# Performance work log

Measured on AMD Instinct MI355X. Metric: run time of the kernel, lower is better.

The kernel has to match this reference:

```python
import jax, jax.numpy as jnp
import numpy as np

B, S, H, UNITS = 32, 2048, 1024, 1024


def setup_inputs() -> dict:
    key = jax.random.key(0)
    ks = jax.random.split(key, 5)
    scale = 1.0 / np.sqrt(H)
    return {
        "query": jax.random.normal(ks[0], (B, H), dtype=jnp.float32),
        "values": jax.random.normal(ks[1], (B, S, H), dtype=jnp.float32),
        "W1": jax.random.normal(ks[2], (H, UNITS), dtype=jnp.float32) * scale,
        "b1": jnp.zeros((UNITS,), dtype=jnp.float32),
        "W2": jax.random.normal(ks[3], (H, UNITS), dtype=jnp.float32) * scale,
        "b2": jnp.zeros((UNITS,), dtype=jnp.float32),
        "V": jax.random.normal(ks[4], (UNITS, 1), dtype=jnp.float32) * (1.0 / np.sqrt(UNITS)),
        "bV": jnp.zeros((1,), dtype=jnp.float32),
    }


def reference(query, values, W1, b1, W2, b2, V, bV):
    # W1(values): [B,S,U]; W2(query): [B,1,U] broadcast over S
    proj_v = jnp.einsum("bsh,hu->bsu", values, W1) + b1
    proj_q = (query @ W2 + b2)[:, None, :]
    score = jnp.tanh(proj_v + proj_q) @ V + bV          # [B,S,1]
    attention_weights = jax.nn.softmax(score, axis=1)   # softmax over seq
    context_vector = jnp.sum(attention_weights * values, axis=1)  # [B,H]
    return (attention_weights, context_vector)
```

## Files before the change

### kernel.cpp

```cpp
#include <hip/hip_runtime.h>
#include <hip/hip_bf16.h>
#include <stdint.h>

#define B_ 32
#define S_ 2048
#define H_ 1024
#define U_ 1024

typedef __attribute__((ext_vector_type(8))) short short8;
typedef __attribute__((ext_vector_type(4))) float f32x4;

#define AS1 __attribute__((address_space(1)))
#define AS3 __attribute__((address_space(3)))

__device__ __forceinline__ unsigned short f2bf(float f) {
  unsigned int u = __float_as_uint(f);
  u += 0x7fffu + ((u >> 16) & 1u);
  return (unsigned short)(u >> 16);
}

__global__ void k_cvt(const float* __restrict__ v, unsigned short* __restrict__ o) {
  const size_t n = (size_t)B_ * S_ * H_;
  const size_t stride = (size_t)gridDim.x * blockDim.x * 8;
  for (size_t i = ((size_t)blockIdx.x * blockDim.x + threadIdx.x) * 8; i < n; i += stride) {
    float4 a = *(const float4*)(v + i), b = *(const float4*)(v + i + 4);
    short8 w;
    w[0]=f2bf(a.x); w[1]=f2bf(a.y); w[2]=f2bf(a.z); w[3]=f2bf(a.w);
    w[4]=f2bf(b.x); w[5]=f2bf(b.y); w[6]=f2bf(b.z); w[7]=f2bf(b.w);
    *(short8*)(o + i) = w;
  }
}

__global__ void k_transpose_w1(const float* __restrict__ W1, unsigned short* __restrict__ W1T) {
  __shared__ float tile[64][65];
  const int tx = threadIdx.x, ty = threadIdx.y;
  const int u0 = blockIdx.x * 64, h0 = blockIdx.y * 64;
#pragma unroll
  for (int i = 0; i < 16; ++i) {
    int hl = ty + i * 4;
    tile[hl][tx] = W1[(size_t)(h0 + hl) * U_ + (u0 + tx)];
  }
  __syncthreads();
#pragma unroll
  for (int i = 0; i < 16; ++i) {
    int ul = ty + i * 4;
    W1T[(size_t)(u0 + ul) * H_ + (h0 + tx)] = f2bf(tile[tx][ul]);
  }
}

__global__ void k_b1q(const float* __restrict__ query, const float* __restrict__ W2,
                      const float* __restrict__ b1, const float* __restrict__ b2,
                      float* __restrict__ b1q) {
  const int b = blockIdx.y;
  const int u = blockIdx.x * 256 + threadIdx.x;
  float acc = b1[u] + b2[u];
  const float* q = query + b * H_;
#pragma unroll 8
  for (int h = 0; h < H_; ++h) acc += q[h] * W2[(size_t)h * U_ + u];
  b1q[b * U_ + u] = acc;
}

#define BM 128
#define BN 256
#define BK 32
#define NSTEP 32

__global__ __launch_bounds__(512, 4)
void k_fused_score(const unsigned short* __restrict__ vbf,
                   const unsigned short* __restrict__ W1T,
                   const float* __restrict__ b1q, const float* __restrict__ V,
                   float* __restrict__ score_part) {
  __shared__ __align__(16) unsigned char smem[49152];
  unsigned short* As = (unsigned short*)smem;
  unsigned short* Bs = (unsigned short*)(smem + 16384);
  float* scorebuf = (float*)smem;

  const int tid = threadIdx.x;
  const int g = blockIdx.x;
  const int seq = (g & 7) * 256 + (g >> 3);
  const int bn = seq & 3;
  const int bm = seq >> 2;

  const int lane = tid & 63, wid = tid >> 6;
  const int wm = wid >> 2, wn = wid & 3;
  const int u0 = bn * BN;

  const int arow_s = tid >> 2;
  const int alc = (tid & 3) ^ ((arow_s >> 1) & 3);
  const unsigned short* aSrc = vbf + (size_t)(bm * BM + arow_s) * H_ + alc * 8;
  const unsigned short* bSrc0 = W1T + (size_t)(u0 + arow_s) * H_ + alc * 8;
  const unsigned short* bSrc1 = bSrc0 + (size_t)128 * H_;

  const int l15 = lane & 15, l16 = lane >> 4;
  const int fsq = ((l16 ^ ((lane >> 1) & 3)) << 3);
  const int pA = (wm * 64 + l15) * 32 + fsq;
  const int pB = (wn * 64 + l15) * 32 + fsq;

  f32x4 acc[4][4];
#pragma unroll
  for (int mf = 0; mf < 4; ++mf)
#pragma unroll
    for (int nf = 0; nf < 4; ++nf) acc[mf][nf] = (f32x4){0.f, 0.f, 0.f, 0.f};

  __builtin_amdgcn_global_load_lds((const AS1 void*)aSrc,
                                   (AS3 void*)&As[tid * 8], 16, 0, 0);
  __builtin_amdgcn_global_load_lds((const AS1 void*)bSrc0,
                                   (AS3 void*)&Bs[tid * 8], 16, 0, 0);
  __builtin_amdgcn_global_load_lds((const AS1 void*)bSrc1,
                                   (AS3 void*)&Bs[4096 + tid * 8], 16, 0, 0);
  __syncthreads();

  int cur = 0;
  for (int t = 0; t < NSTEP; ++t) {
    if (t + 1 < NSTEP) {
      const int ko = (t + 1) * BK;
      __builtin_amdgcn_global_load_lds((const AS1 void*)(aSrc + ko),
                                       (AS3 void*)&As[(cur ^ 1) * 4096 + tid * 8], 16, 0, 0);
      __builtin_amdgcn_global_load_lds((const AS1 void*)(bSrc0 + ko),
                                       (AS3 void*)&Bs[(cur ^ 1) * 8192 + tid * 8], 16, 0, 0);
      __builtin_amdgcn_global_load_lds((const AS1 void*)(bSrc1 + ko),
                                       (AS3 void*)&Bs[(cur ^ 1) * 8192 + 4096 + tid * 8], 16, 0, 0);
    }
    short8 af[4], bv[4];
#pragma unroll
    for (int mf = 0; mf < 4; ++mf)
      af[mf] = *(const short8*)&As[cur * 4096 + pA + mf * 512];
#pragma unroll
    for (int nf = 0; nf < 4; ++nf)
      bv[nf] = *(const short8*)&Bs[cur * 8192 + pB + nf * 512];
#pragma unroll
    for (int nf = 0; nf < 4; ++nf)
#pragma unroll
      for (int mf = 0; mf < 4; ++mf)
        acc[mf][nf] = __builtin_amdgcn_mfma_f32_16x16x32_bf16(af[mf], bv[nf], acc[mf][nf], 0, 0, 0);
    __syncthreads();
    cur ^= 1;
  }

  const int b_blk = bm >> 4;
  float bqv[4], vvv[4];
#pragma unroll
  for (int nf = 0; nf < 4; ++nf) {
    const int ug = u0 + wn * 64 + nf * 16 + l15;
    bqv[nf] = b1q[b_blk * U_ + ug];
    vvv[nf] = V[ug];
  }
  float rp[4][4];
#pragma unroll
  for (int mf = 0; mf < 4; ++mf)
#pragma unroll
    for (int j = 0; j < 4; ++j) rp[mf][j] = 0.f;
#pragma unroll
  for (int nf = 0; nf < 4; ++nf)
#pragma unroll
    for (int mf = 0; mf < 4; ++mf) {
      const f32x4 c = acc[mf][nf];
#pragma unroll
      for (int j = 0; j < 4; ++j) {
        const float x = c[j] + bqv[nf];
        const float e = __expf(2.f * x);
        const float tt = 1.f - 2.f / (e + 1.f);
        rp[mf][j] += tt * vvv[nf];
      }
    }
#pragma unroll
  for (int mf = 0; mf < 4; ++mf)
#pragma unroll
    for (int j = 0; j < 4; ++j) {
      float v = rp[mf][j];
      v += __shfl_xor(v, 1);
      v += __shfl_xor(v, 2);
      v += __shfl_xor(v, 4);
      v += __shfl_xor(v, 8);
      rp[mf][j] = v;
    }
  if (l15 == 0) {
#pragma unroll
    for (int mf = 0; mf < 4; ++mf)
#pragma unroll
      for (int j = 0; j < 4; ++j)
        scorebuf[(wm * 64 + mf * 16 + l16 * 4 + j) * 4 + wn] = rp[mf][j];
  }
  __syncthreads();
  if (tid < BM) {
    const float s = scorebuf[tid * 4 + 0] + scorebuf[tid * 4 + 1] +
                    scorebuf[tid * 4 + 2] + scorebuf[tid * 4 + 3];
    score_part[(size_t)bn * (B_ * S_) + bm * BM + tid] = s;
  }
}

__global__ void k_softmax(const float* __restrict__ sp, float* __restrict__ aw) {
  __shared__ float red[8];
  const int b = blockIdx.x, tid = threadIdx.x;
  const int BS = B_ * S_;
  float x[8];
  float m = -1e30f;
#pragma unroll
  for (int i = 0; i < 8; ++i) {
    const int s = b * S_ + tid + i * 256;
    x[i] = sp[s] + sp[BS + s] + sp[2 * BS + s] + sp[3 * BS + s];
    m = fmaxf(m, x[i]);
  }
#pragma unroll
  for (int off = 32; off; off >>= 1) m = fmaxf(m, __shfl_xor(m, off));
  if ((tid & 63) == 0) red[tid >> 6] = m;
  __syncthreads();
  m = fmaxf(fmaxf(red[0], red[1]), fmaxf(red[2], red[3]));
  float e[8];
  float sum = 0.f;
#pragma unroll
  for (int i = 0; i < 8; ++i) { e[i] = __expf(x[i] - m); sum += e[i]; }
#pragma unroll
  for (int off = 32; off; off >>= 1) sum += __shfl_xor(sum, off);
  __syncthreads();
  if ((tid & 63) == 0) red[4 + (tid >> 6)] = sum;
  __syncthreads();
  sum = red[4] + red[5] + red[6] + red[7];
  const float inv = 1.f / sum;
#pragma unroll
  for (int i = 0; i < 8; ++i) aw[b * S_ + tid + i * 256] = e[i] * inv;
}

__global__ void k_ctx_partial(const float* __restrict__ values, const float* __restrict__ aw,
                              float* __restrict__ part) {
  __shared__ float a_s[128];
  const int b = blockIdx.y, sc = blockIdx.x, tid = threadIdx.x;
  if (tid < 128) a_s[tid] = aw[b * S_ + sc * 128 + tid];
  __syncthreads();
  const float4* vp = (const float4*)values + (size_t)(b * S_ + sc * 128) * (H_ / 4) + tid;
  float4 acc = {0.f, 0.f, 0.f, 0.f};
#pragma unroll 4
  for (int i = 0; i < 128; ++i) {
    const float4 v = vp[(size_t)i * (H_ / 4)];
    const float a = a_s[i];
    acc.x += a * v.x; acc.y += a * v.y; acc.z += a * v.z; acc.w += a * v.w;
  }
  ((float4*)part)[(size_t)(b * 16 + sc) * (H_ / 4) + tid] = acc;
}

__global__ void k_ctx_combine(const float* __restrict__ part, float* __restrict__ ctx) {
  const int b = blockIdx.x, tid = threadIdx.x;
  float4 s = {0.f, 0.f, 0.f, 0.f};
#pragma unroll
  for (int c = 0; c < 16; ++c) {
    const float4 v = ((const float4*)part)[(size_t)(b * 16 + c) * (H_ / 4) + tid];
    s.x += v.x; s.y += v.y; s.z += v.z; s.w += v.w;
  }
  ((float4*)ctx)[b * (H_ / 4) + tid] = s;
}

extern "C" void kernel_launch(void* const* d_in, const int* in_sizes, int n_in,
                              void* d_out, int out_size, void* d_ws, size_t ws_size,
                              hipStream_t stream) {
  const float* query  = (const float*)d_in[0];
  const float* values = (const float*)d_in[1];
  const float* W1     = (const float*)d_in[2];
  const float* b1     = (const float*)d_in[3];
  const float* W2     = (const float*)d_in[4];
  const float* b2     = (const float*)d_in[5];
  const float* V      = (const float*)d_in[6];

  char* ws = (char*)d_ws;
  unsigned short* W1T = (unsigned short*)ws;
  float* b1q   = (float*)(ws + 2u * 1024u * 1024u);
  float* spart = (float*)(ws + 2u * 1024u * 1024u + 128u * 1024u);
  float* cpart = (float*)(ws + 2u * 1024u * 1024u + 128u * 1024u + 1024u * 1024u);
  unsigned short* vbf = (unsigned short*)(ws + 8u * 1024u * 1024u);

  float* aw  = (float*)d_out;
  float* ctx = aw + B_ * S_;

  k_transpose_w1<<<dim3(16, 16), dim3(64, 4), 0, stream>>>(W1, W1T);
  k_b1q<<<dim3(4, 32), dim3(256), 0, stream>>>(query, W2, b1, b2, b1q);
  k_cvt<<<dim3(2048), dim3(256), 0, stream>>>(values, vbf);
  k_fused_score<<<dim3(2048), dim3(512), 0, stream>>>(vbf, W1T, b1q, V, spart);
  k_softmax<<<dim3(32), dim3(256), 0, stream>>>(spart, aw);
  k_ctx_partial<<<dim3(16, 32), dim3(256), 0, stream>>>(values, aw, cpart);
  k_ctx_combine<<<dim3(32), dim3(256), 0, stream>>>(cpart, ctx);
}
```

Before: 342.0 us.

## Triple-buffer GEMM loads, batch query projection, read bf16 values for context

The fused score GEMM moves from double to triple buffering of its LDS tiles. Prefetch runs two steps ahead, with explicit vmcnt waits and raw barriers in place of __syncthreads, to hide global load latency. The query projection is split into a shared-memory tiled partial kernel plus a combine kernel, so W2 is read once for all batches. The context reduction now reads the bf16 copy of values instead of fp32, halving its traffic at some cost in precision. The larger LDS footprint (72KB) may reduce blocks per CU.

```diff
diff --git a/kernel.cpp b/kernel.cpp
--- a/kernel.cpp
+++ b/kernel.cpp
@@ -12,11 +12,15 @@
 
 #define AS1 __attribute__((address_space(1)))
 #define AS3 __attribute__((address_space(3)))
+#define FENCE __builtin_amdgcn_sched_barrier(0)
 
 __device__ __forceinline__ unsigned short f2bf(float f) {
   unsigned int u = __float_as_uint(f);
   u += 0x7fffu + ((u >> 16) & 1u);
   return (unsigned short)(u >> 16);
+}
+__device__ __forceinline__ float bf2f(unsigned short s) {
+  return __uint_as_float(((unsigned int)s) << 16);
 }
 
 __global__ void k_cvt(const float* __restrict__ v, unsigned short* __restrict__ o) {
@@ -48,16 +52,36 @@
   }
 }
 
-__global__ void k_b1q(const float* __restrict__ query, const float* __restrict__ W2,
-                      const float* __restrict__ b1, const float* __restrict__ b2,
-                      float* __restrict__ b1q) {
+__global__ void k_b1q_part(const float* __restrict__ query, const float* __restrict__ W2,
+                           float* __restrict__ qpart) {
+  __shared__ float q_sh[32 * 128];
+  const int u = blockIdx.x * 256 + threadIdx.x;
+  const int hs = blockIdx.y;
+  for (int i = threadIdx.x; i < 4096; i += 256) {
+    const int b = i >> 7, h = i & 127;
+    q_sh[i] = query[b * H_ + hs * 128 + h];
+  }
+  __syncthreads();
+  float acc[32];
+#pragma unroll
+  for (int b = 0; b < 32; ++b) acc[b] = 0.f;
+  for (int h = 0; h < 128; ++h) {
+    const float w = W2[(size_t)(hs * 128 + h) * U_ + u];
+#pragma unroll
+    for (int b = 0; b < 32; ++b) acc[b] += q_sh[b * 128 + h] * w;
+  }
+#pragma unroll
+  for (int b = 0; b < 32; ++b) qpart[((size_t)hs * 32 + b) * U_ + u] = acc[b];
+}
+
+__global__ void k_b1q_comb(const float* __restrict__ qpart, const float* __restrict__ b1,
+                           const float* __restrict__ b2, float* __restrict__ b1q) {
+  const int u = blockIdx.x * 256 + threadIdx.x;
   const int b = blockIdx.y;
-  const int u = blockIdx.x * 256 + threadIdx.x;
-  float acc = b1[u] + b2[u];
-  const float* q = query + b * H_;
-#pragma unroll 8
-  for (int h = 0; h < H_; ++h) acc += q[h] * W2[(size_t)h * U_ + u];
-  b1q[b * U_ + u] = acc;
+  float s = b1[u] + b2[u];
+#pragma unroll
+  for (int hs = 0; hs < 8; ++hs) s += qpart[((size_t)hs * 32 + b) * U_ + u];
+  b1q[b * U_ + u] = s;
 }
 
 #define BM 128
@@ -70,9 +94,9 @@
                    const unsigned short* __restrict__ W1T,
                    const float* __restrict__ b1q, const float* __restrict__ V,
                    float* __restrict__ score_part) {
-  __shared__ __align__(16) unsigned char smem[49152];
+  __shared__ __align__(16) unsigned char smem[73728];
   unsigned short* As = (unsigned short*)smem;
-  unsigned short* Bs = (unsigned short*)(smem + 16384);
+  unsigned short* Bs = (unsigned short*)(smem + 24576);
   float* scorebuf = (float*)smem;
 
   const int tid = threadIdx.x;
@@ -102,41 +126,47 @@
 #pragma unroll
     for (int nf = 0; nf < 4; ++nf) acc[mf][nf] = (f32x4){0.f, 0.f, 0.f, 0.f};
 
-  __builtin_amdgcn_global_load_lds((const AS1 void*)aSrc,
-                                   (AS3 void*)&As[tid * 8], 16, 0, 0);
-  __builtin_amdgcn_global_load_lds((const AS1 void*)bSrc0,
-                                   (AS3 void*)&Bs[tid * 8], 16, 0, 0);
-  __builtin_amdgcn_global_load_lds((const AS1 void*)bSrc1,
-                                   (AS3 void*)&Bs[4096 + tid * 8], 16, 0, 0);
-  __syncthreads();
-
-  int cur = 0;
+#define STAGE(tt, slot) { \
+    const int ko_ = (tt) * BK; \
+    __builtin_amdgcn_global_load_lds((const AS1 void*)(aSrc + ko_), \
+        (AS3 void*)&As[(slot) * 4096 + tid * 8], 16, 0, 0); \
+    __builtin_amdgcn_global_load_lds((const AS1 void*)(bSrc0 + ko_), \
+        (AS3 void*)&Bs[(slot) * 8192 + tid * 8], 16, 0, 0); \
+    __builtin_amdgcn_global_load_lds((const AS1 void*)(bSrc1 + ko_), \
+        (AS3 void*)&Bs[(slot) * 8192 + 4096 + tid * 8], 16, 0, 0); }
+
+  STAGE(0, 0);
+  STAGE(1, 1);
+  asm volatile("s_waitcnt vmcnt(3)" ::: "memory");
+  FENCE;
+  __builtin_amdgcn_s_barrier();
+
+  int slot = 0;
   for (int t = 0; t < NSTEP; ++t) {
-    if (t + 1 < NSTEP) {
-      const int ko = (t + 1) * BK;
-      __builtin_amdgcn_global_load_lds((const AS1 void*)(aSrc + ko),
-                                       (AS3 void*)&As[(cur ^ 1) * 4096 + tid * 8], 16, 0, 0);
-      __builtin_amdgcn_global_load_lds((const AS1 void*)(bSrc0 + ko),
-                                       (AS3 void*)&Bs[(cur ^ 1) * 8192 + tid * 8], 16, 0, 0);
-      __builtin_amdgcn_global_load_lds((const AS1 void*)(bSrc1 + ko),
-                                       (AS3 void*)&Bs[(cur ^ 1) * 8192 + 4096 + tid * 8], 16, 0, 0);
-    }
+    const int nslot = (slot >= 1) ? slot - 1 : 2;
+    if (t + 2 < NSTEP) { STAGE(t + 2, nslot); }
+    FENCE;
     short8 af[4], bv[4];
 #pragma unroll
     for (int mf = 0; mf < 4; ++mf)
-      af[mf] = *(const short8*)&As[cur * 4096 + pA + mf * 512];
+      af[mf] = *(const short8*)&As[slot * 4096 + pA + mf * 512];
 #pragma unroll
     for (int nf = 0; nf < 4; ++nf)
-      bv[nf] = *(const short8*)&Bs[cur * 8192 + pB + nf * 512];
+      bv[nf] = *(const short8*)&Bs[slot * 8192 + pB + nf * 512];
 #pragma unroll
     for (int nf = 0; nf < 4; ++nf)
 #pragma unroll
       for (int mf = 0; mf < 4; ++mf)
         acc[mf][nf] = __builtin_amdgcn_mfma_f32_16x16x32_bf16(af[mf], bv[nf], acc[mf][nf], 0, 0, 0);
-    __syncthreads();
-    cur ^= 1;
-  }
-
+    FENCE;
+    if (t + 2 < NSTEP) { asm volatile("s_waitcnt vmcnt(3)" ::: "memory"); }
+    else               { asm volatile("s_waitcnt vmcnt(0)" ::: "memory"); }
+    FENCE;
+    __builtin_amdgcn_s_barrier();
+    slot = (slot == 2) ? 0 : slot + 1;
+  }
+
+  __syncthreads();
   const int b_blk = bm >> 4;
   float bqv[4], vvv[4];
 #pragma unroll
@@ -221,19 +251,20 @@
   for (int i = 0; i < 8; ++i) aw[b * S_ + tid + i * 256] = e[i] * inv;
 }
 
-__global__ void k_ctx_partial(const float* __restrict__ values, const float* __restrict__ aw,
+__global__ void k_ctx_partial(const unsigned short* __restrict__ vbf, const float* __restrict__ aw,
                               float* __restrict__ part) {
   __shared__ float a_s[128];
   const int b = blockIdx.y, sc = blockIdx.x, tid = threadIdx.x;
   if (tid < 128) a_s[tid] = aw[b * S_ + sc * 128 + tid];
   __syncthreads();
-  const float4* vp = (const float4*)values + (size_t)(b * S_ + sc * 128) * (H_ / 4) + tid;
+  const unsigned short* vp = vbf + (size_t)(b * S_ + sc * 128) * H_ + tid * 4;
   float4 acc = {0.f, 0.f, 0.f, 0.f};
 #pragma unroll 4
   for (int i = 0; i < 128; ++i) {
-    const float4 v = vp[(size_t)i * (H_ / 4)];
+    const ushort4 v = *(const ushort4*)(vp + (size_t)i * H_);
     const float a = a_s[i];
-    acc.x += a * v.x; acc.y += a * v.y; acc.z += a * v.z; acc.w += a * v.w;
+    acc.x += a * bf2f(v.x); acc.y += a * bf2f(v.y);
+    acc.z += a * bf2f(v.z); acc.w += a * bf2f(v.w);
   }
   ((float4*)part)[(size_t)(b * 16 + sc) * (H_ / 4) + tid] = acc;
 }
@@ -264,17 +295,19 @@
   unsigned short* W1T = (unsigned short*)ws;
   float* b1q   = (float*)(ws + 2u * 1024u * 1024u);
   float* spart = (float*)(ws + 2u * 1024u * 1024u + 128u * 1024u);
-  float* cpart = (float*)(ws + 2u * 1024u * 1024u + 128u * 1024u + 1024u * 1024u);
+  float* cpart = (float*)(ws + 3u * 1024u * 1024u + 128u * 1024u);
+  float* qpart = (float*)(ws + 5u * 1024u * 1024u + 128u * 1024u);
   unsigned short* vbf = (unsigned short*)(ws + 8u * 1024u * 1024u);
 
   float* aw  = (float*)d_out;
   float* ctx = aw + B_ * S_;
 
   k_transpose_w1<<<dim3(16, 16), dim3(64, 4), 0, stream>>>(W1, W1T);
-  k_b1q<<<dim3(4, 32), dim3(256), 0, stream>>>(query, W2, b1, b2, b1q);
+  k_b1q_part<<<dim3(4, 8), dim3(256), 0, stream>>>(query, W2, qpart);
+  k_b1q_comb<<<dim3(4, 32), dim3(256), 0, stream>>>(qpart, b1, b2, b1q);
   k_cvt<<<dim3(2048), dim3(256), 0, stream>>>(values, vbf);
   k_fused_score<<<dim3(2048), dim3(512), 0, stream>>>(vbf, W1T, b1q, V, spart);
   k_softmax<<<dim3(32), dim3(256), 0, stream>>>(spart, aw);
-  k_ctx_partial<<<dim3(16, 32), dim3(256), 0, stream>>>(values, aw, cpart);
+  k_ctx_partial<<<dim3(16, 32), dim3(256), 0, stream>>>(vbf, aw, cpart);
   k_ctx_combine<<<dim3(32), dim3(256), 0, stream>>>(cpart, ctx);
 }
```

New measurement: 310.0 us. 1.1x faster.
